# Performance work log

Measured on AMD Instinct MI355X. Metric: run time of the kernel, lower is better.

## Reference

```python
import jax, jax.numpy as jnp
import numpy as np

B, S, N = 8, 4096, 512
K_DIM, HEADS, WS = 512, 8, 128
HD = K_DIM // HEADS


def setup_inputs() -> dict:
    key = jax.random.key(0)
    ks = jax.random.split(key, 9)
    sc = 0.02
    return {
        "inputs": jax.random.normal(ks[0], (B, S, N), dtype=jnp.float32),
        "Wq": jax.random.normal(ks[1], (K_DIM, N), dtype=jnp.float32) * sc,
        "bq": jax.random.normal(ks[2], (K_DIM,), dtype=jnp.float32) * sc,
        "Wk": jax.random.normal(ks[3], (K_DIM, N), dtype=jnp.float32) * sc,
        "bk": jax.random.normal(ks[4], (K_DIM,), dtype=jnp.float32) * sc,
        "Wv": jax.random.normal(ks[5], (K_DIM, N), dtype=jnp.float32) * sc,
        "bv": jax.random.normal(ks[6], (K_DIM,), dtype=jnp.float32) * sc,
        "Wp": jax.random.normal(ks[7], (N, K_DIM), dtype=jnp.float32) * sc,
        "bp": jax.random.normal(ks[8], (N,), dtype=jnp.float32) * sc,
    }


def reference(inputs, Wq, bq, Wk, bk, Wv, bv, Wp, bp):
    b, s, n = inputs.shape
    nw = s // WS  # number of windows per sequence
    # QKV projections (torch Linear: x @ W.T + b)
    q = inputs @ Wq.T + bq  # [B,S,K]
    k = inputs @ Wk.T + bk
    v = inputs @ Wv.T + bv

    def to_windows(t):
        # [B,S,K] -> [B*nw, H, WS, HD]
        t = t.reshape(b * nw, WS, HEADS, HD)
        return t.transpose(0, 2, 1, 3)

    q, k, v = to_windows(q), to_windows(k), to_windows(v)
    scale = HD ** (-0.5)
    # windowed attention: [BW,H,WS,WS]
    score = jnp.einsum('whqd,whkd->whqk', q, k) * scale
    attn = jax.nn.softmax(score, axis=-1)  # dropout is identity in eval
    out = jnp.einsum('whqk,whkd->whqd', attn, v)  # [BW,H,WS,HD]
    out = out.transpose(0, 2, 1, 3).reshape(b, s, K_DIM)  # window reverse
    out = out @ Wp.T + bp  # [B,S,N]
    return out
```

## Files before the change

### kernel.cpp

```cpp
#include <hip/hip_runtime.h>
#include <hip/hip_bf16.h>
#include <stdint.h>


typedef __bf16 bf16;
typedef __bf16 bf16x8 __attribute__((ext_vector_type(8)));
typedef __bf16 bf16x4 __attribute__((ext_vector_type(4)));
typedef __bf16 bf16x2 __attribute__((ext_vector_type(2)));
typedef float  f32x4  __attribute__((ext_vector_type(4)));

#define DEV static __device__ __forceinline__

DEV void gld_lds16(const bf16* g, bf16* l) {
  __builtin_amdgcn_global_load_lds(
      (__attribute__((address_space(1))) void*)(g),
      (__attribute__((address_space(3))) void*)(l), 16, 0, 0);
}

__global__ void cast_all(const float* __restrict__ x,
                         const float* __restrict__ Wq, const float* __restrict__ Wk,
                         const float* __restrict__ Wv, const float* __restrict__ Wp,
                         bf16* __restrict__ xb, bf16* __restrict__ wb) {
  int i = blockIdx.x * blockDim.x + threadIdx.x;
  const float* src;
  bf16* dst;
  if (i < 4194304) {
    src = x + i * 4;
    dst = xb + i * 4;
  } else {
    int e = (i - 4194304) * 4;
    int off;
    const float* w;
    if (e < 786432) {
      int seg = e >> 18;
      off = e & 262143;
      w = (seg == 0) ? Wq : ((seg == 1) ? Wk : Wv);
    } else {
      off = e - 786432;
      w = Wp;
    }
    src = w + off;
    dst = wb + e;
  }
  float4 v = *(const float4*)src;
  bf16x4 o;
  o[0] = (bf16)v.x; o[1] = (bf16)v.y; o[2] = (bf16)v.z; o[3] = (bf16)v.w;
  *(bf16x4*)dst = o;
}

template <bool BF16OUT, int NTILES>
__global__ __launch_bounds__(512, 2)
void gemm256f(const bf16* __restrict__ A, const bf16* __restrict__ B,
              const float* __restrict__ bias0, const float* __restrict__ bias1,
              const float* __restrict__ bias2, void* __restrict__ Cout) {
  constexpr int Ntot = NTILES * 256;
  constexpr int NK = 8;
  __shared__ __align__(16) bf16 smem[2][2][256 * 64];

  const int tid = threadIdx.x;
  const int wave = tid >> 6, lane = tid & 63;
  const int wm = wave >> 2, wn = wave & 3;
  const int lane15 = lane & 15, kq = lane >> 4;
  const int srow = lane >> 3, sg = (lane & 7) ^ srow;

  const int nb = gridDim.x;
  const int j = blockIdx.x;
  const int l = (j & 7) * (nb >> 3) + (j >> 3);
  const long row0 = (long)(l / NTILES) * 256;
  const long col0 = (long)(l % NTILES) * 256;

  f32x4 acc[8][4] = {};
  bf16x8 af0[4][2], af1[4][2], bq0[2][2], bq1[2][2];

#define STG_A(T, BUF, I)                                                       \
  gld_lds16(A + (row0 + wave * 32 + (I) * 8 + srow) * 512 + (long)(T) * 64 +   \
                sg * 8,                                                        \
            &smem[BUF][0][(wave * 32 + (I) * 8) * 64]);
#define STG_B(T, BUF, I)                                                       \
  gld_lds16(B + (col0 + wave * 32 + (I) * 8 + srow) * 512 + (long)(T) * 64 +   \
                sg * 8,                                                        \
            &smem[BUF][1][(wave * 32 + (I) * 8) * 64]);

#define READ_A(DST, QM, BUF)                                                   \
  {                                                                            \
    _Pragma("unroll") for (int mt_ = 0; mt_ < 4; ++mt_) {                      \
      const int r_ = wm * 128 + (QM) * 64 + mt_ * 16 + lane15;                 \
      const bf16* p_ = &smem[BUF][0][r_ * 64];                                 \
      _Pragma("unroll") for (int ks_ = 0; ks_ < 2; ++ks_) {                    \
        const int c_ = (ks_ * 4 + kq) ^ (r_ & 7);                              \
        DST[mt_][ks_] = *(const bf16x8*)(p_ + c_ * 8);                         \
      }                                                                        \
    }                                                                          \
  }

#define READ_B(DST, QN, BUF)                                                   \
  {                                                                            \
    _Pragma("unroll") for (int nt_ = 0; nt_ < 2; ++nt_) {                      \
      const int r_ = wn * 64 + (QN) * 32 + nt_ * 16 + lane15;                  \
      const bf16* p_ = &smem[BUF][1][r_ * 64];                                 \
      _Pragma("unroll") for (int ks_ = 0; ks_ < 2; ++ks_) {                    \
        const int c_ = (ks_ * 4 + kq) ^ (r_ & 7);                              \
        DST[nt_][ks_] = *(const bf16x8*)(p_ + c_ * 8);                         \
      }                                                                        \
    }                                                                          \
  }

#define MMA_Q(AF, BF, QM, QN)                                                  \
  {                                                                            \
    __builtin_amdgcn_s_setprio(1);                                             \
    _Pragma("unroll") for (int ks_ = 0; ks_ < 2; ++ks_)                        \
    _Pragma("unroll") for (int mt_ = 0; mt_ < 4; ++mt_)                        \
    _Pragma("unroll") for (int nt_ = 0; nt_ < 2; ++nt_)                        \
      acc[(QM) * 4 + mt_][(QN) * 2 + nt_] =                                    \
          __builtin_amdgcn_mfma_f32_16x16x32_bf16(                             \
              AF[mt_][ks_], BF[nt_][ks_],                                      \
              acc[(QM) * 4 + mt_][(QN) * 2 + nt_], 0, 0, 0);                   \
    __builtin_amdgcn_s_setprio(0);                                             \
  }

  {
    STG_A(0, 0, 0) STG_A(0, 0, 1) STG_A(0, 0, 2) STG_A(0, 0, 3)
    STG_B(0, 0, 0) STG_B(0, 0, 1) STG_B(0, 0, 2) STG_B(0, 0, 3)
  }
  asm volatile("s_waitcnt vmcnt(0)" ::: "memory");
  __builtin_amdgcn_s_barrier();

  for (int kk = 0; kk < NK; ++kk) {
    const int cur = kk & 1, nxt = cur ^ 1;
    const bool st = (kk + 1 < NK);
    if (st) {
      STG_A(kk + 1, nxt, 0) STG_A(kk + 1, nxt, 1)
      STG_A(kk + 1, nxt, 2) STG_A(kk + 1, nxt, 3)
      STG_B(kk + 1, nxt, 0) STG_B(kk + 1, nxt, 1)
      STG_B(kk + 1, nxt, 2) STG_B(kk + 1, nxt, 3)
    }
    READ_A(af0, 0, cur);
    READ_B(bq0, 0, cur);
    __builtin_amdgcn_s_barrier();
    MMA_Q(af0, bq0, 0, 0);
    __builtin_amdgcn_s_barrier();
    READ_B(bq1, 1, cur);
    __builtin_amdgcn_s_barrier();
    MMA_Q(af0, bq1, 0, 1);
    __builtin_amdgcn_s_barrier();
    READ_A(af1, 1, cur);
    __builtin_amdgcn_s_barrier();
    MMA_Q(af1, bq1, 1, 1);
    MMA_Q(af1, bq0, 1, 0);
    if (st) {
      asm volatile("s_waitcnt vmcnt(0)" ::: "memory");
      __builtin_amdgcn_s_barrier();
    }
  }

#undef STG_A
#undef STG_B
#undef READ_A
#undef READ_B
#undef MMA_Q

  const long crow = row0 + wm * 128;
  const long ccol = col0 + wn * 64;
  for (int m = 0; m < 8; ++m) {
    for (int n = 0; n < 4; ++n) {
      const long col = ccol + n * 16 + lane15;
      const float* bsel;
      if (NTILES == 6) {
        const int seg = (int)(col >> 9);
        bsel = (seg == 0) ? bias0 : ((seg == 1) ? bias1 : bias2);
      } else {
        bsel = bias0;
      }
      const float bias = bsel[col & 511];
      const long row = crow + m * 16 + kq * 4;
      for (int g = 0; g < 4; ++g) {
        const float v = acc[m][n][g] + bias;
        if (BF16OUT) ((bf16*)Cout)[(row + g) * Ntot + col] = (bf16)v;
        else         ((float*)Cout)[(row + g) * Ntot + col] = v;
      }
    }
  }
}

__global__ __launch_bounds__(512, 4)
void attn_win(const bf16* __restrict__ QKV, bf16* __restrict__ Out) {
  __shared__ __align__(16) char smem[49152];
  bf16* Qs = (bf16*)smem;
  bf16* Ks = Qs + 128 * 64;
  bf16* Ps = (bf16*)smem;
  bf16* Vt = (bf16*)(smem + 32768);
  bf16* Os = (bf16*)smem;

  const int tid = threadIdx.x;
  const int wave = tid >> 6, lane = tid & 63;
  const int lane15 = lane & 15, quad = lane >> 4;
  const int win = blockIdx.x >> 3, head = blockIdx.x & 7;

  const bf16* Qg = QKV + (size_t)win * 128 * 1536 + head * 64;
  const bf16* Kg = Qg + 512;
  const bf16* Vg = Qg + 1024;

  {
    const int srow = lane >> 3;
    const int sg = (lane & 7) ^ srow;
    for (int i = 0; i < 2; ++i) {
      int r0 = (wave * 2 + i) * 8;
      gld_lds16(Qg + (size_t)(r0 + srow) * 1536 + sg * 8, Qs + r0 * 64 + lane * 8);
      gld_lds16(Kg + (size_t)(r0 + srow) * 1536 + sg * 8, Ks + r0 * 64 + lane * 8);
    }
  }
  {
    int tp = tid >> 3;
    int d0 = (tid & 7) * 8;
    bf16x8 v0 = *(const bf16x8*)(Vg + (size_t)(2 * tp) * 1536 + d0);
    bf16x8 v1 = *(const bf16x8*)(Vg + (size_t)(2 * tp + 1) * 1536 + d0);
    int gt = tp >> 2, po = tp & 3;
    for (int j = 0; j < 8; ++j) {
      int d = d0 + j;
      int p = gt ^ ((d >> 3) ^ (d & 7));
      bf16x2 pr;
      pr[0] = v0[j]; pr[1] = v1[j];
      *(bf16x2*)(Vt + d * 128 + p * 8 + po * 2) = pr;
    }
  }
  __syncthreads();

  f32x4 accs[8] = {};
  {
    bf16x8 aq[2];
    for (int s = 0; s < 2; ++s) {
      int row = wave * 16 + lane15;
      aq[s] = *(const bf16x8*)(Qs + row * 64 + (((s * 4 + quad) ^ (lane15 & 7)) * 8));
    }
    for (int c = 0; c < 8; ++c) {
      int row = c * 16 + lane15;
      for (int s = 0; s < 2; ++s) {
        bf16x8 bk = *(const bf16x8*)(Ks + row * 64 + (((s * 4 + quad) ^ (lane15 & 7)) * 8));
        accs[c] = __builtin_amdgcn_mfma_f32_16x16x32_bf16(aq[s], bk, accs[c], 0, 0, 0);
      }
    }
  }
  __syncthreads();

  const float scale = 0.125f;
  for (int g = 0; g < 4; ++g) {
    float sum = 0.f;
    for (int c = 0; c < 8; ++c) {
      float e = __expf(accs[c][g] * scale);
      accs[c][g] = e;
      sum += e;
    }
    for (int mk = 1; mk <= 8; mk <<= 1) sum += __shfl_xor(sum, mk, 64);
    float inv = 1.0f / sum;
    int prow = wave * 16 + quad * 4 + g;
    int rsw = prow & 7;
    for (int c = 0; c < 8; ++c) {
      int col = c * 16 + lane15;
      int p = (col >> 3) ^ rsw;
      Ps[prow * 128 + p * 8 + (col & 7)] = (bf16)(accs[c][g] * inv);
    }
  }
  __syncthreads();

  f32x4 acco[4] = {};
  for (int kk = 0; kk < 4; ++kk) {
    int arow = wave * 16 + lane15;
    int pa = (kk * 4 + quad) ^ (arow & 7);
    bf16x8 a = *(const bf16x8*)(Ps + arow * 128 + pa * 8);
    for (int c = 0; c < 4; ++c) {
      int d = c * 16 + lane15;
      int p = (kk * 4 + quad) ^ ((d >> 3) ^ (d & 7));
      bf16x8 b = *(const bf16x8*)(Vt + d * 128 + p * 8);
      acco[c] = __builtin_amdgcn_mfma_f32_16x16x32_bf16(a, b, acco[c], 0, 0, 0);
    }
  }

  __syncthreads();
  {
    int rowb = wave * 16 + quad * 4;
    for (int c = 0; c < 4; ++c) {
      int col = c * 16 + lane15;
      for (int g = 0; g < 4; ++g)
        Os[(rowb + g) * 64 + col] = (bf16)acco[c][g];
    }
  }
  __syncthreads();
  {
    bf16* Og = Out + (size_t)win * 128 * 512 + head * 64;
    for (int i = 0; i < 2; ++i) {
      int idx = tid + i * 512;
      int r = idx >> 3, ch = idx & 7;
      bf16x8 v = *(const bf16x8*)(Os + r * 64 + ch * 8);
      *(bf16x8*)(Og + (size_t)r * 512 + ch * 8) = v;
    }
  }
}

extern "C" void kernel_launch(void* const* d_in, const int* in_sizes, int n_in,
                              void* d_out, int out_size, void* d_ws, size_t ws_size,
                              hipStream_t stream) {
  const float* x  = (const float*)d_in[0];
  const float* Wq = (const float*)d_in[1];
  const float* bq = (const float*)d_in[2];
  const float* Wk = (const float*)d_in[3];
  const float* bk = (const float*)d_in[4];
  const float* Wv = (const float*)d_in[5];
  const float* bv = (const float*)d_in[6];
  const float* Wp = (const float*)d_in[7];
  const float* bp = (const float*)d_in[8];

  bf16* Xb    = (bf16*)d_ws;
  bf16* Wqkvb = Xb + 16777216;
  bf16* Wpb   = Wqkvb + 786432;
  bf16* QKVb  = Wpb + 262144;
  bf16* AttnB = QKVb + 50331648;

  cast_all<<<17408, 256, 0, stream>>>(x, Wq, Wk, Wv, Wp, Xb, Wqkvb);
  gemm256f<true, 6><<<768, 512, 0, stream>>>(Xb, Wqkvb, bq, bk, bv, QKVb);
  attn_win<<<2048, 512, 0, stream>>>(QKVb, AttnB);
  gemm256f<false, 2><<<256, 512, 0, stream>>>(AttnB, Wpb, bp, bp, bp, d_out);
}
```

Before: 246.7 us.

## Fuse fp32-to-bf16 input cast into QKV GEMM A-tile staging

Removes the separate cast of the large fp32 input tensor. The QKV GEMM now loads fp32 A tiles into registers, converts them to bf16 and writes them to LDS itself, so only the weights are still cast in a smaller pre-kernel. It also spreads the async LDS staging loads across the three MMA phases instead of issuing them all at the top of each iteration. The cost is that each QKV block rereads fp32 A (twice the bytes of bf16) for every one of its 6 column tiles. It also adds register pressure and synchronous LDS writes in the GEMM main loop.

```diff
diff --git a/kernel.cpp b/kernel.cpp
--- a/kernel.cpp
+++ b/kernel.cpp
@@ -17,51 +17,46 @@
       (__attribute__((address_space(3))) void*)(l), 16, 0, 0);
 }
 
-__global__ void cast_all(const float* __restrict__ x,
-                         const float* __restrict__ Wq, const float* __restrict__ Wk,
-                         const float* __restrict__ Wv, const float* __restrict__ Wp,
-                         bf16* __restrict__ xb, bf16* __restrict__ wb) {
+__global__ void cast_w(const float* __restrict__ Wq, const float* __restrict__ Wk,
+                       const float* __restrict__ Wv, const float* __restrict__ Wp,
+                       bf16* __restrict__ wb) {
   int i = blockIdx.x * blockDim.x + threadIdx.x;
-  const float* src;
-  bf16* dst;
-  if (i < 4194304) {
-    src = x + i * 4;
-    dst = xb + i * 4;
+  int e = i * 4;
+  int off;
+  const float* w;
+  if (e < 786432) {
+    int seg = e >> 18;
+    off = e & 262143;
+    w = (seg == 0) ? Wq : ((seg == 1) ? Wk : Wv);
   } else {
-    int e = (i - 4194304) * 4;
-    int off;
-    const float* w;
-    if (e < 786432) {
-      int seg = e >> 18;
-      off = e & 262143;
-      w = (seg == 0) ? Wq : ((seg == 1) ? Wk : Wv);
-    } else {
-      off = e - 786432;
-      w = Wp;
-    }
-    src = w + off;
-    dst = wb + e;
-  }
-  float4 v = *(const float4*)src;
+    off = e - 786432;
+    w = Wp;
+  }
+  float4 v = *(const float4*)(w + off);
   bf16x4 o;
   o[0] = (bf16)v.x; o[1] = (bf16)v.y; o[2] = (bf16)v.z; o[3] = (bf16)v.w;
-  *(bf16x4*)dst = o;
-}
-
-template <bool BF16OUT, int NTILES>
+  *(bf16x4*)(wb + e) = o;
+}
+
+template <bool CASTA, bool BF16OUT, int NTILES>
 __global__ __launch_bounds__(512, 2)
-void gemm256f(const bf16* __restrict__ A, const bf16* __restrict__ B,
+void gemm256f(const void* __restrict__ Aptr, const bf16* __restrict__ B,
               const float* __restrict__ bias0, const float* __restrict__ bias1,
               const float* __restrict__ bias2, void* __restrict__ Cout) {
   constexpr int Ntot = NTILES * 256;
   constexpr int NK = 8;
   __shared__ __align__(16) bf16 smem[2][2][256 * 64];
 
+  const float* Af = (const float*)Aptr;
+  const bf16*  Ab = (const bf16*)Aptr;
+
   const int tid = threadIdx.x;
   const int wave = tid >> 6, lane = tid & 63;
   const int wm = wave >> 2, wn = wave & 3;
   const int lane15 = lane & 15, kq = lane >> 4;
-  const int srow = lane >> 3, sg = (lane & 7) ^ srow;
+  const int srow = lane >> 3;
+  const int c8 = lane & 7;
+  const int sg = c8 ^ srow;
 
   const int nb = gridDim.x;
   const int j = blockIdx.x;
@@ -71,15 +66,39 @@
 
   f32x4 acc[8][4] = {};
   bf16x8 af0[4][2], af1[4][2], bq0[2][2], bq1[2][2];
+  float4 areg[8];
 
 #define STG_A(T, BUF, I)                                                       \
-  gld_lds16(A + (row0 + wave * 32 + (I) * 8 + srow) * 512 + (long)(T) * 64 +   \
+  gld_lds16(Ab + (row0 + wave * 32 + (I) * 8 + srow) * 512 + (long)(T) * 64 +  \
                 sg * 8,                                                        \
             &smem[BUF][0][(wave * 32 + (I) * 8) * 64]);
 #define STG_B(T, BUF, I)                                                       \
   gld_lds16(B + (col0 + wave * 32 + (I) * 8 + srow) * 512 + (long)(T) * 64 +   \
                 sg * 8,                                                        \
             &smem[BUF][1][(wave * 32 + (I) * 8) * 64]);
+
+#define A_LOADF(T)                                                             \
+  {                                                                            \
+    const long kb_ = (long)(T) * 64;                                           \
+    _Pragma("unroll") for (int i_ = 0; i_ < 4; ++i_) {                         \
+      const float* p_ =                                                        \
+          Af + (row0 + wave * 32 + i_ * 8 + srow) * 512 + kb_ + c8 * 8;        \
+      areg[2 * i_]     = *(const float4*)(p_);                                 \
+      areg[2 * i_ + 1] = *(const float4*)(p_ + 4);                             \
+    }                                                                          \
+  }
+#define A_WRITEF(BUF)                                                          \
+  {                                                                            \
+    _Pragma("unroll") for (int i_ = 0; i_ < 4; ++i_) {                         \
+      bf16x8 o_;                                                               \
+      o_[0] = (bf16)areg[2 * i_].x;     o_[1] = (bf16)areg[2 * i_].y;          \
+      o_[2] = (bf16)areg[2 * i_].z;     o_[3] = (bf16)areg[2 * i_].w;          \
+      o_[4] = (bf16)areg[2 * i_ + 1].x; o_[5] = (bf16)areg[2 * i_ + 1].y;      \
+      o_[6] = (bf16)areg[2 * i_ + 1].z; o_[7] = (bf16)areg[2 * i_ + 1].w;      \
+      *(bf16x8*)(&smem[BUF][0][(wave * 32 + i_ * 8 + srow) * 64 + sg * 8]) =   \
+          o_;                                                                  \
+    }                                                                          \
+  }
 
 #define READ_A(DST, QM, BUF)                                                   \
   {                                                                            \
@@ -118,43 +137,64 @@
     __builtin_amdgcn_s_setprio(0);                                             \
   }
 
-  {
+  if constexpr (CASTA) {
+    A_LOADF(0)
+    STG_B(0, 0, 0) STG_B(0, 0, 1) STG_B(0, 0, 2) STG_B(0, 0, 3)
+    A_WRITEF(0)
+    asm volatile("s_waitcnt vmcnt(0) lgkmcnt(0)" ::: "memory");
+  } else {
     STG_A(0, 0, 0) STG_A(0, 0, 1) STG_A(0, 0, 2) STG_A(0, 0, 3)
     STG_B(0, 0, 0) STG_B(0, 0, 1) STG_B(0, 0, 2) STG_B(0, 0, 3)
-  }
-  asm volatile("s_waitcnt vmcnt(0)" ::: "memory");
+    asm volatile("s_waitcnt vmcnt(0)" ::: "memory");
+  }
   __builtin_amdgcn_s_barrier();
 
   for (int kk = 0; kk < NK; ++kk) {
     const int cur = kk & 1, nxt = cur ^ 1;
     const bool st = (kk + 1 < NK);
     if (st) {
-      STG_A(kk + 1, nxt, 0) STG_A(kk + 1, nxt, 1)
-      STG_A(kk + 1, nxt, 2) STG_A(kk + 1, nxt, 3)
-      STG_B(kk + 1, nxt, 0) STG_B(kk + 1, nxt, 1)
-      STG_B(kk + 1, nxt, 2) STG_B(kk + 1, nxt, 3)
+      if constexpr (CASTA) { A_LOADF(kk + 1) }
     }
     READ_A(af0, 0, cur);
     READ_B(bq0, 0, cur);
+    if (st) {
+      if constexpr (CASTA) { STG_B(kk + 1, nxt, 0) STG_B(kk + 1, nxt, 1) }
+      else { STG_A(kk + 1, nxt, 0) STG_A(kk + 1, nxt, 1) STG_B(kk + 1, nxt, 0) }
+    }
     __builtin_amdgcn_s_barrier();
     MMA_Q(af0, bq0, 0, 0);
     __builtin_amdgcn_s_barrier();
     READ_B(bq1, 1, cur);
+    if (st) {
+      if constexpr (CASTA) { STG_B(kk + 1, nxt, 2) }
+      else { STG_A(kk + 1, nxt, 2) STG_A(kk + 1, nxt, 3) STG_B(kk + 1, nxt, 1) }
+    }
     __builtin_amdgcn_s_barrier();
     MMA_Q(af0, bq1, 0, 1);
     __builtin_amdgcn_s_barrier();
     READ_A(af1, 1, cur);
+    if (st) {
+      if constexpr (CASTA) { STG_B(kk + 1, nxt, 3) }
+      else { STG_B(kk + 1, nxt, 2) STG_B(kk + 1, nxt, 3) }
+    }
     __builtin_amdgcn_s_barrier();
     MMA_Q(af1, bq1, 1, 1);
     MMA_Q(af1, bq0, 1, 0);
     if (st) {
-      asm volatile("s_waitcnt vmcnt(0)" ::: "memory");
+      if constexpr (CASTA) {
+        A_WRITEF(nxt)
+        asm volatile("s_waitcnt vmcnt(0) lgkmcnt(0)" ::: "memory");
+      } else {
+        asm volatile("s_waitcnt vmcnt(0)" ::: "memory");
+      }
       __builtin_amdgcn_s_barrier();
     }
   }
 
 #undef STG_A
 #undef STG_B
+#undef A_LOADF
+#undef A_WRITEF
 #undef READ_A
 #undef READ_B
 #undef MMA_Q
@@ -315,8 +355,8 @@
   bf16* QKVb  = Wpb + 262144;
   bf16* AttnB = QKVb + 50331648;
 
-  cast_all<<<17408, 256, 0, stream>>>(x, Wq, Wk, Wv, Wp, Xb, Wqkvb);
-  gemm256f<true, 6><<<768, 512, 0, stream>>>(Xb, Wqkvb, bq, bk, bv, QKVb);
+  cast_w<<<1024, 256, 0, stream>>>(Wq, Wk, Wv, Wp, Wqkvb);
+  gemm256f<true, true, 6><<<768, 512, 0, stream>>>(x, Wqkvb, bq, bk, bv, QKVb);
   attn_win<<<2048, 512, 0, stream>>>(QKVb, AttnB);
-  gemm256f<false, 2><<<256, 512, 0, stream>>>(AttnB, Wpb, bp, bp, bp, d_out);
-}
+  gemm256f<false, false, 2><<<256, 512, 0, stream>>>(AttnB, Wpb, bp, bp, bp, d_out);
+}
```

Measured after the change: 266.2 us. +7.9%, slower.
